# Kernel optimization log

Measured on AMD Instinct MI355X. Metric: run time of the kernel, lower is better.

The kernel has to match this reference:

```python
import jax, jax.numpy as jnp
import numpy as np

RADIUS = 5
WIN = (RADIUS - 1) * 2 + 1  # 9


def setup_inputs() -> dict:
    key = jax.random.key(0)
    k1, k2 = jax.random.split(key)
    B, K, H, W = 4, 4, 224, 224
    seg = jax.random.uniform(k1, (B, K, H, W), dtype=jnp.float32)
    weight = jax.random.uniform(k2, (B, 1, H, W, WIN, WIN), dtype=jnp.float32)
    return {"seg": seg, "weight": weight}


def reference(seg, weight):
    # seg: [B,K,H,W]; weight: [B,1,H,W,w,w] local affinity window, w = 2*(radius-1)+1
    B, K, H, W = seg.shape
    Kconst = jnp.float32(K)
    # torch pads by `radius` on all sides but only uses window offsets 0..2*(radius-1),
    # i.e. relative offsets [-radius, radius-2] -- replicate exactly.
    padded = jnp.pad(seg, ((0, 0), (0, 0), (RADIUS, RADIUS), (RADIUS, RADIUS)))
    # weighted sum over the local window without materializing [B,K,H,W,w,w]
    sum_w_seg = jnp.zeros_like(seg)
    for m in range(WIN):
        for n in range(WIN):
            sum_w_seg = sum_w_seg + padded[:, :, m:m + H, n:n + W] * weight[:, :, :, :, m, n]
    assocA = jnp.sum(sum_w_seg * seg, axis=(-1, -2))                      # [B,K]
    assocV = jnp.sum(jnp.sum(weight, axis=(-1, -2)) * seg, axis=(-1, -2))  # [B,K]
    assoc = jnp.sum(assocA / assocV, axis=-1)                              # [B]
    return jnp.sum(Kconst - assoc)
```

## Files before the change

### kernel.cpp

```cpp
#include <hip/hip_runtime.h>

#define RADIUS 5
#define WIN 9
#define BB 4
#define KK 4
#define HH 224
#define WW 224
#define HW (HH * WW)
#define PD 234
#define PAREA (PD * PD)
#define NBUCKET 64
#define PARTIAL_FLOATS (NBUCKET * BB * 8)
#define BLOCKS_PER_B (HW / 64)
#define TOTAL_BLOCKS (BB * BLOCKS_PER_B)


__global__ __launch_bounds__(256) void ncuts_pad(
    const float* __restrict__ seg, float4* __restrict__ pseg, float* __restrict__ zr)
{
    const int tid = blockIdx.x * 256 + threadIdx.x;
    if (tid < PARTIAL_FLOATS) zr[tid] = 0.f;
    if (tid >= BB * PAREA) return;
    const int b  = tid / PAREA;
    const int rc = tid - b * PAREA;
    const int r  = rc / PD;
    const int c  = rc - r * PD;
    const int hh = r - RADIUS;
    const int ww = c - RADIUS;
    float4 v = {0.f, 0.f, 0.f, 0.f};
    if (hh >= 0 && hh < HH && ww >= 0 && ww < WW) {
        const float* sb = seg + (size_t)b * KK * HW + hh * WW + ww;
        v.x = sb[0 * HW];
        v.y = sb[1 * HW];
        v.z = sb[2 * HW];
        v.w = sb[3 * HW];
    }
    pseg[tid] = v;
}

__global__ __launch_bounds__(64) void ncuts_main(
    const float* __restrict__ weight,
    const float4* __restrict__ pseg,
    float* __restrict__ partial)
{
    __shared__ float wlds[64 * 81];

    const int lane = threadIdx.x;
    const int tid  = blockIdx.x * 64 + lane;
    const int b    = tid / HW;
    const int rem  = tid - b * HW;
    const int h    = rem / WW;
    const int w    = rem - h * WW;

    const float4* wsrc = (const float4*)(weight + (size_t)blockIdx.x * (64 * 81));
    float4* ldsb = (float4*)wlds;
    #pragma unroll
    for (int j = 0; j < 20; ++j)
        __builtin_amdgcn_global_load_lds(
            (__attribute__((address_space(1))) void*)(wsrc + j * 64 + lane),
            (__attribute__((address_space(3))) void*)(ldsb + j * 64),
            16, 0, 0);
    if (lane < 16)
        __builtin_amdgcn_global_load_lds(
            (__attribute__((address_space(1))) void*)(wsrc + 1280 + lane),
            (__attribute__((address_space(3))) void*)(ldsb + 1280),
            16, 0, 0);

    const float4* p4 = pseg + (size_t)b * PAREA;
    const float4 t = p4[(h + RADIUS) * PD + (w + RADIUS)];

    __syncthreads();

    const float* wl = &wlds[lane * 81];

    float a0 = 0.f, a1 = 0.f, a2 = 0.f, a3 = 0.f, wsum = 0.f;

    #pragma unroll
    for (int m = 0; m < WIN; ++m) {
        const int base = (h + m) * PD + w;
        #pragma unroll
        for (int n = 0; n < WIN; ++n) {
            const float wv = wl[m * WIN + n];
            const float4 s = p4[base + n];
            a0 = fmaf(wv, s.x, a0);
            a1 = fmaf(wv, s.y, a1);
            a2 = fmaf(wv, s.z, a2);
            a3 = fmaf(wv, s.w, a3);
            wsum += wv;
        }
    }

    float vals[8] = { a0 * t.x, a1 * t.y, a2 * t.z, a3 * t.w,
                      wsum * t.x, wsum * t.y, wsum * t.z, wsum * t.w };

    #pragma unroll
    for (int i = 0; i < 8; ++i) {
        float v = vals[i];
        v += __shfl_down(v, 32);
        v += __shfl_down(v, 16);
        v += __shfl_down(v, 8);
        v += __shfl_down(v, 4);
        v += __shfl_down(v, 2);
        v += __shfl_down(v, 1);
        vals[i] = v;
    }

    if (lane == 0) {
        const int bb     = blockIdx.x - b * BLOCKS_PER_B;
        const int bucket = bb & (NBUCKET - 1);
        float* dst = partial + (bucket * BB + b) * 8;
        #pragma unroll
        for (int i = 0; i < 8; ++i)
            atomicAdd(dst + i, vals[i]);
    }
}

__global__ __launch_bounds__(64) void ncuts_final(
    const float* __restrict__ partial, float* __restrict__ out)
{
    __shared__ float sums[32];
    const int t = threadIdx.x;
    if (t < 32) {
        float s = 0.f;
        for (int bucket = 0; bucket < NBUCKET; ++bucket)
            s += partial[bucket * 32 + t];
        sums[t] = s;
    }
    __syncthreads();
    if (t == 0) {
        float total = 0.f;
        for (int b = 0; b < BB; ++b) {
            float assoc = 0.f;
            for (int k = 0; k < KK; ++k) {
                const float A = sums[b * 8 + k];
                const float V = sums[b * 8 + 4 + k];
                assoc += A / V;
            }
            total += (float)KK - assoc;
        }
        out[0] = total;
    }
}

extern "C" void kernel_launch(void* const* d_in, const int* in_sizes, int n_in,
                              void* d_out, int out_size, void* d_ws, size_t ws_size,
                              hipStream_t stream) {
    const float* seg    = (const float*)d_in[0];
    const float* weight = (const float*)d_in[1];
    float* out     = (float*)d_out;
    float* wsf     = (float*)d_ws;
    float* partial = wsf;
    float4* pseg   = (float4*)(wsf + PARTIAL_FLOATS);

    {
        const int total = BB * PAREA;
        const int grid  = (total + 255) / 256;
        hipLaunchKernelGGL(ncuts_pad, dim3(grid), dim3(256), 0, stream, seg, pseg, wsf);
    }

    hipLaunchKernelGGL(ncuts_main, dim3(TOTAL_BLOCKS), dim3(64), 0, stream,
                       weight, pseg, partial);

    hipLaunchKernelGGL(ncuts_final, dim3(1), dim3(64), 0, stream, partial, out);
}
```

Baseline: 105.7 us.

## Stream weight elements linearly per lane instead of staging per-pixel windows in LDS

The main kernel now treats the weight tensor as a flat stream: each lane reads one float per step with fully coalesced accesses and derives the pixel and window offset by incremental index tracking, instead of staging each pixel's 81 weights in LDS. The center seg value is folded into each weight before accumulation, so both numerator and denominator sums are built per element. Blocks grow to 4 waves, each covering 28 steps of 64 elements. The aim is to drop LDS staging and the barrier and to make the dominant weight read purely sequential. In exchange every step does two gather loads of seg (center and neighbor), recomputes the window offset with a divide by 9, and runs a branchy index update.

Result: slower. 114.8 us (+8.6%).

```diff
diff --git a/kernel.cpp b/kernel.cpp
--- a/kernel.cpp
+++ b/kernel.cpp
@@ -11,7 +11,12 @@
 #define PAREA (PD * PD)
 #define NBUCKET 64
 #define PARTIAL_FLOATS (NBUCKET * BB * 8)
-#define BLOCKS_PER_B (HW / 64)
+#define ELEMS_PER_B (HW * 81)
+#define STEPS 28
+#define WAVE_ELEMS (64 * STEPS)
+#define BLOCK_WAVES 4
+#define BLOCK_ELEMS (BLOCK_WAVES * WAVE_ELEMS)
+#define BLOCKS_PER_B (ELEMS_PER_B / BLOCK_ELEMS)
 #define TOTAL_BLOCKS (BB * BLOCKS_PER_B)
 
 
@@ -38,61 +43,60 @@
     pseg[tid] = v;
 }
 
-__global__ __launch_bounds__(64) void ncuts_main(
+__global__ __launch_bounds__(256) void ncuts_main(
     const float* __restrict__ weight,
     const float4* __restrict__ pseg,
     float* __restrict__ partial)
 {
-    __shared__ float wlds[64 * 81];
+    const int lane = threadIdx.x & 63;
+    const int wid  = threadIdx.x >> 6;
+    const int b    = blockIdx.x / BLOCKS_PER_B;
+    const int blkb = blockIdx.x - b * BLOCKS_PER_B;
 
-    const int lane = threadIdx.x;
-    const int tid  = blockIdx.x * 64 + lane;
-    const int b    = tid / HW;
-    const int rem  = tid - b * HW;
-    const int h    = rem / WW;
-    const int w    = rem - h * WW;
+    const unsigned wave_base = (unsigned)(blkb * BLOCK_WAVES + wid) * WAVE_ELEMS;
+    const unsigned idx0 = wave_base + (unsigned)lane;
 
-    const float4* wsrc = (const float4*)(weight + (size_t)blockIdx.x * (64 * 81));
-    float4* ldsb = (float4*)wlds;
-    #pragma unroll
-    for (int j = 0; j < 20; ++j)
-        __builtin_amdgcn_global_load_lds(
-            (__attribute__((address_space(1))) void*)(wsrc + j * 64 + lane),
-            (__attribute__((address_space(3))) void*)(ldsb + j * 64),
-            16, 0, 0);
-    if (lane < 16)
-        __builtin_amdgcn_global_load_lds(
-            (__attribute__((address_space(1))) void*)(wsrc + 1280 + lane),
-            (__attribute__((address_space(3))) void*)(ldsb + 1280),
-            16, 0, 0);
+    const float*  wsrc = weight + (size_t)b * ELEMS_PER_B;
+    const float4* p4   = pseg   + (size_t)b * PAREA;
 
-    const float4* p4 = pseg + (size_t)b * PAREA;
-    const float4 t = p4[(h + RADIUS) * PD + (w + RADIUS)];
+    unsigned p = idx0 / 81u;
+    unsigned o = idx0 - p * 81u;
+    unsigned h = p / 224u;
+    unsigned w = p - h * 224u;
 
-    __syncthreads();
-
-    const float* wl = &wlds[lane * 81];
-
-    float a0 = 0.f, a1 = 0.f, a2 = 0.f, a3 = 0.f, wsum = 0.f;
+    float a0 = 0.f, a1 = 0.f, a2 = 0.f, a3 = 0.f;
+    float v0 = 0.f, v1 = 0.f, v2 = 0.f, v3 = 0.f;
 
     #pragma unroll
-    for (int m = 0; m < WIN; ++m) {
-        const int base = (h + m) * PD + w;
-        #pragma unroll
-        for (int n = 0; n < WIN; ++n) {
-            const float wv = wl[m * WIN + n];
-            const float4 s = p4[base + n];
-            a0 = fmaf(wv, s.x, a0);
-            a1 = fmaf(wv, s.y, a1);
-            a2 = fmaf(wv, s.z, a2);
-            a3 = fmaf(wv, s.w, a3);
-            wsum += wv;
+    for (int j = 0; j < STEPS; ++j) {
+        const float wv = wsrc[wave_base + j * 64 + lane];
+
+        const unsigned m = o / 9u;
+        const unsigned n = o - m * 9u;
+
+        const float4 sc = p4[(h + RADIUS) * PD + (w + RADIUS)];
+        const float4 sv = p4[(h + m) * PD + (w + n)];
+
+        const float w0 = wv * sc.x;
+        const float w1 = wv * sc.y;
+        const float w2 = wv * sc.z;
+        const float w3 = wv * sc.w;
+
+        a0 = fmaf(w0, sv.x, a0);
+        a1 = fmaf(w1, sv.y, a1);
+        a2 = fmaf(w2, sv.z, a2);
+        a3 = fmaf(w3, sv.w, a3);
+        v0 += w0; v1 += w1; v2 += w2; v3 += w3;
+
+        o += 64u;
+        if (o >= 81u) {
+            o -= 81u;
+            ++w;
+            if (w == 224u) { w = 0u; ++h; }
         }
     }
 
-    float vals[8] = { a0 * t.x, a1 * t.y, a2 * t.z, a3 * t.w,
-                      wsum * t.x, wsum * t.y, wsum * t.z, wsum * t.w };
-
+    float vals[8] = { a0, a1, a2, a3, v0, v1, v2, v3 };
     #pragma unroll
     for (int i = 0; i < 8; ++i) {
         float v = vals[i];
@@ -106,8 +110,7 @@
     }
 
     if (lane == 0) {
-        const int bb     = blockIdx.x - b * BLOCKS_PER_B;
-        const int bucket = bb & (NBUCKET - 1);
+        const int bucket = (blkb + wid * 16) & (NBUCKET - 1);
         float* dst = partial + (bucket * BB + b) * 8;
         #pragma unroll
         for (int i = 0; i < 8; ++i)
@@ -158,7 +161,7 @@
         hipLaunchKernelGGL(ncuts_pad, dim3(grid), dim3(256), 0, stream, seg, pseg, wsf);
     }
 
-    hipLaunchKernelGGL(ncuts_main, dim3(TOTAL_BLOCKS), dim3(64), 0, stream,
+    hipLaunchKernelGGL(ncuts_main, dim3(TOTAL_BLOCKS), dim3(256), 0, stream,
                        weight, pseg, partial);
 
     hipLaunchKernelGGL(ncuts_final, dim3(1), dim3(64), 0, stream, partial, out);
```

## Process multiple row tiles per wave with double-buffered async LDS staging

Applied to the files above, without the earlier changes.

Each 64-lane block now handles seven 56-pixel row-segment tiles. It double-buffers both the weight window and a 9x64 padded seg patch in LDS using global_load_lds, with manual vmcnt waits, so the next tile's loads overlap the current tile's FMAs. Seg neighbours are read from LDS instead of global/L1, and the atomic reductions drop by a factor of seven. In exchange, 8 of 64 lanes sit idle, each block uses more LDS, there are fewer blocks in flight, and correctness depends on the hand-counted waitcnt values.

Measured after the change: 109.9 us. 4.0% more time.

```diff
diff --git a/kernel.cpp b/kernel.cpp
--- a/kernel.cpp
+++ b/kernel.cpp
@@ -11,8 +11,18 @@
 #define PAREA (PD * PD)
 #define NBUCKET 64
 #define PARTIAL_FLOATS (NBUCKET * BB * 8)
-#define BLOCKS_PER_B (HW / 64)
-#define TOTAL_BLOCKS (BB * BLOCKS_PER_B)
+
+#define TILE_PIX 56
+#define TILES_PER_B (HH * 4)
+#define TOTAL_TILES (BB * TILES_PER_B)
+#define TPB 7
+#define NBLK (TOTAL_TILES / TPB)
+#define TW_FLOATS (TILE_PIX * 81)
+#define TW_BYTES (TW_FLOATS * 4)
+#define TW_FULL_LOADS 17
+#define TW_REM 46
+#define TP_BYTES (9 * 64 * 16)
+#define LDS_BYTES (2 * TW_BYTES + 2 * TP_BYTES)
 
 
 __global__ __launch_bounds__(256) void ncuts_pad(
@@ -43,56 +53,96 @@
     const float4* __restrict__ pseg,
     float* __restrict__ partial)
 {
-    __shared__ float wlds[64 * 81];
+    __shared__ char lds[LDS_BYTES];
 
     const int lane = threadIdx.x;
-    const int tid  = blockIdx.x * 64 + lane;
-    const int b    = tid / HW;
-    const int rem  = tid - b * HW;
-    const int h    = rem / WW;
-    const int w    = rem - h * WW;
-
-    const float4* wsrc = (const float4*)(weight + (size_t)blockIdx.x * (64 * 81));
-    float4* ldsb = (float4*)wlds;
-    #pragma unroll
-    for (int j = 0; j < 20; ++j)
-        __builtin_amdgcn_global_load_lds(
-            (__attribute__((address_space(1))) void*)(wsrc + j * 64 + lane),
-            (__attribute__((address_space(3))) void*)(ldsb + j * 64),
-            16, 0, 0);
-    if (lane < 16)
-        __builtin_amdgcn_global_load_lds(
-            (__attribute__((address_space(1))) void*)(wsrc + 1280 + lane),
-            (__attribute__((address_space(3))) void*)(ldsb + 1280),
-            16, 0, 0);
-
+    const int blk  = blockIdx.x;
+    const int t0   = blk * TPB;
+    const int b    = t0 / TILES_PER_B;
     const float4* p4 = pseg + (size_t)b * PAREA;
-    const float4 t = p4[(h + RADIUS) * PD + (w + RADIUS)];
-
-    __syncthreads();
-
-    const float* wl = &wlds[lane * 81];
-
-    float a0 = 0.f, a1 = 0.f, a2 = 0.f, a3 = 0.f, wsum = 0.f;
-
-    #pragma unroll
-    for (int m = 0; m < WIN; ++m) {
-        const int base = (h + m) * PD + w;
+
+    auto stage_w = [&](int t, int s) {
+        const float4* src = (const float4*)(weight + (size_t)t * TW_FLOATS);
+        char* dst = lds + s * TW_BYTES;
         #pragma unroll
-        for (int n = 0; n < WIN; ++n) {
-            const float wv = wl[m * WIN + n];
-            const float4 s = p4[base + n];
-            a0 = fmaf(wv, s.x, a0);
-            a1 = fmaf(wv, s.y, a1);
-            a2 = fmaf(wv, s.z, a2);
-            a3 = fmaf(wv, s.w, a3);
-            wsum += wv;
+        for (int j = 0; j < TW_FULL_LOADS; ++j)
+            __builtin_amdgcn_global_load_lds(
+                (__attribute__((address_space(1))) void*)(src + j * 64 + lane),
+                (__attribute__((address_space(3))) void*)(dst + j * 1024),
+                16, 0, 0);
+        if (lane < TW_REM)
+            __builtin_amdgcn_global_load_lds(
+                (__attribute__((address_space(1))) void*)(src + TW_FULL_LOADS * 64 + lane),
+                (__attribute__((address_space(3))) void*)(dst + TW_FULL_LOADS * 1024),
+                16, 0, 0);
+    };
+    auto stage_p = [&](int t, int s) {
+        const int r  = t - b * TILES_PER_B;
+        const int h  = r >> 2;
+        const int w0 = (r & 3) * TILE_PIX;
+        const float4* src = p4 + h * PD + w0;
+        char* dst = lds + 2 * TW_BYTES + s * TP_BYTES;
+        #pragma unroll
+        for (int rr = 0; rr < 9; ++rr)
+            __builtin_amdgcn_global_load_lds(
+                (__attribute__((address_space(1))) void*)(src + rr * PD + lane),
+                (__attribute__((address_space(3))) void*)(dst + rr * 1024),
+                16, 0, 0);
+    };
+
+    stage_w(t0 + 0, 0);
+    stage_p(t0 + 0, 0);
+    stage_w(t0 + 1, 1);
+    stage_p(t0 + 1, 1);
+
+    float accA0 = 0.f, accA1 = 0.f, accA2 = 0.f, accA3 = 0.f;
+    float accV0 = 0.f, accV1 = 0.f, accV2 = 0.f, accV3 = 0.f;
+
+    for (int i = 0; i < TPB; ++i) {
+        if (i < TPB - 1) asm volatile("s_waitcnt vmcnt(27)" ::: "memory");
+        else             asm volatile("s_waitcnt vmcnt(0)"  ::: "memory");
+        __builtin_amdgcn_sched_barrier(0);
+
+        const int s = i & 1;
+        const float*  wl = (const float*)(lds + s * TW_BYTES) + lane * 81;
+        const float4* pl = (const float4*)(lds + 2 * TW_BYTES + s * TP_BYTES) + lane;
+
+        if (lane < TILE_PIX) {
+            float a0 = 0.f, a1 = 0.f, a2 = 0.f, a3 = 0.f, ws = 0.f;
+            #pragma unroll
+            for (int m = 0; m < WIN; ++m) {
+                #pragma unroll
+                for (int n = 0; n < WIN; ++n) {
+                    const float  wv = wl[m * WIN + n];
+                    const float4 sv = pl[m * 64 + n];
+                    a0 = fmaf(wv, sv.x, a0);
+                    a1 = fmaf(wv, sv.y, a1);
+                    a2 = fmaf(wv, sv.z, a2);
+                    a3 = fmaf(wv, sv.w, a3);
+                    ws += wv;
+                }
+            }
+            const float4 sc = pl[5 * 64 + 5];
+            accA0 = fmaf(a0, sc.x, accA0);
+            accA1 = fmaf(a1, sc.y, accA1);
+            accA2 = fmaf(a2, sc.z, accA2);
+            accA3 = fmaf(a3, sc.w, accA3);
+            accV0 = fmaf(ws, sc.x, accV0);
+            accV1 = fmaf(ws, sc.y, accV1);
+            accV2 = fmaf(ws, sc.z, accV2);
+            accV3 = fmaf(ws, sc.w, accV3);
         }
-    }
-
-    float vals[8] = { a0 * t.x, a1 * t.y, a2 * t.z, a3 * t.w,
-                      wsum * t.x, wsum * t.y, wsum * t.z, wsum * t.w };
-
+
+        if (i + 2 < TPB) {
+            __builtin_amdgcn_sched_barrier(0);
+            asm volatile("s_waitcnt lgkmcnt(0)" ::: "memory");
+            __builtin_amdgcn_sched_barrier(0);
+            stage_w(t0 + i + 2, s);
+            stage_p(t0 + i + 2, s);
+        }
+    }
+
+    float vals[8] = { accA0, accA1, accA2, accA3, accV0, accV1, accV2, accV3 };
     #pragma unroll
     for (int i = 0; i < 8; ++i) {
         float v = vals[i];
@@ -104,10 +154,8 @@
         v += __shfl_down(v, 1);
         vals[i] = v;
     }
-
     if (lane == 0) {
-        const int bb     = blockIdx.x - b * BLOCKS_PER_B;
-        const int bucket = bb & (NBUCKET - 1);
+        const int bucket = blk & (NBUCKET - 1);
         float* dst = partial + (bucket * BB + b) * 8;
         #pragma unroll
         for (int i = 0; i < 8; ++i)
@@ -158,7 +206,7 @@
         hipLaunchKernelGGL(ncuts_pad, dim3(grid), dim3(256), 0, stream, seg, pseg, wsf);
     }
 
-    hipLaunchKernelGGL(ncuts_main, dim3(TOTAL_BLOCKS), dim3(64), 0, stream,
+    hipLaunchKernelGGL(ncuts_main, dim3(NBLK), dim3(64), 0, stream,
                        weight, pseg, partial);
 
     hipLaunchKernelGGL(ncuts_final, dim3(1), dim3(64), 0, stream, partial, out);
```

## Split each pixel's window across two lanes with 32-pixel row segments per block

Applied to the files above, without the earlier changes.

Each 64-lane block now covers 32 pixels of one row instead of 64 pixels, and each pixel's 9x9 window is split between two lanes by even and odd column offsets. This doubles the number of blocks and halves the LDS staged per block, which is meant to raise occupancy and shorten each lane's serial FMA and load chain. The cost is twice as many blocks, wave-level reductions and atomics, plus a lane-divergent ninth column.

Result: slower. 115.6 us (+9.3%).

```diff
diff --git a/kernel.cpp b/kernel.cpp
--- a/kernel.cpp
+++ b/kernel.cpp
@@ -11,8 +11,15 @@
 #define PAREA (PD * PD)
 #define NBUCKET 64
 #define PARTIAL_FLOATS (NBUCKET * BB * 8)
-#define BLOCKS_PER_B (HW / 64)
-#define TOTAL_BLOCKS (BB * BLOCKS_PER_B)
+
+#define SEGPIX 32
+#define SEGS_PER_ROW 7
+#define SEGS_PER_B (HH * SEGS_PER_ROW)
+#define NBLK (BB * SEGS_PER_B)
+#define WSEG_FLOATS (SEGPIX * 81)
+#define WSEG_BYTES (WSEG_FLOATS * 4)
+#define WSEG_FULL 10
+#define WSEG_REM_LANES 8
 
 
 __global__ __launch_bounds__(256) void ncuts_pad(
@@ -43,55 +50,67 @@
     const float4* __restrict__ pseg,
     float* __restrict__ partial)
 {
-    __shared__ float wlds[64 * 81];
+    __shared__ float wlds[WSEG_FLOATS];
 
     const int lane = threadIdx.x;
-    const int tid  = blockIdx.x * 64 + lane;
-    const int b    = tid / HW;
-    const int rem  = tid - b * HW;
-    const int h    = rem / WW;
-    const int w    = rem - h * WW;
+    const int blk  = blockIdx.x;
+    const int b    = blk / SEGS_PER_B;
+    const int sb   = blk - b * SEGS_PER_B;
+    const int h    = sb / SEGS_PER_ROW;
+    const int w0   = (sb - h * SEGS_PER_ROW) * SEGPIX;
+    const int q    = lane >> 1;
+    const int z    = lane & 1;
 
-    const float4* wsrc = (const float4*)(weight + (size_t)blockIdx.x * (64 * 81));
+    const float4* wsrc = (const float4*)(weight + (size_t)blk * WSEG_FLOATS);
     float4* ldsb = (float4*)wlds;
     #pragma unroll
-    for (int j = 0; j < 20; ++j)
+    for (int j = 0; j < WSEG_FULL; ++j)
         __builtin_amdgcn_global_load_lds(
             (__attribute__((address_space(1))) void*)(wsrc + j * 64 + lane),
             (__attribute__((address_space(3))) void*)(ldsb + j * 64),
             16, 0, 0);
-    if (lane < 16)
+    if (lane < WSEG_REM_LANES)
         __builtin_amdgcn_global_load_lds(
-            (__attribute__((address_space(1))) void*)(wsrc + 1280 + lane),
-            (__attribute__((address_space(3))) void*)(ldsb + 1280),
+            (__attribute__((address_space(1))) void*)(wsrc + WSEG_FULL * 64 + lane),
+            (__attribute__((address_space(3))) void*)(ldsb + WSEG_FULL * 64),
             16, 0, 0);
 
     const float4* p4 = pseg + (size_t)b * PAREA;
-    const float4 t = p4[(h + RADIUS) * PD + (w + RADIUS)];
+    const float4 t = p4[(h + RADIUS) * PD + (w0 + q + RADIUS)];
 
     __syncthreads();
 
-    const float* wl = &wlds[lane * 81];
+    const float* wl = wlds + q * 81;
 
-    float a0 = 0.f, a1 = 0.f, a2 = 0.f, a3 = 0.f, wsum = 0.f;
+    float a0 = 0.f, a1 = 0.f, a2 = 0.f, a3 = 0.f, ws = 0.f;
 
     #pragma unroll
     for (int m = 0; m < WIN; ++m) {
-        const int base = (h + m) * PD + w;
+        const int rowbase = (h + m) * PD + w0 + q;
         #pragma unroll
-        for (int n = 0; n < WIN; ++n) {
-            const float wv = wl[m * WIN + n];
-            const float4 s = p4[base + n];
-            a0 = fmaf(wv, s.x, a0);
-            a1 = fmaf(wv, s.y, a1);
-            a2 = fmaf(wv, s.z, a2);
-            a3 = fmaf(wv, s.w, a3);
-            wsum += wv;
+        for (int j = 0; j < 4; ++j) {
+            const int n = 2 * j + z;
+            const float  wv = wl[m * WIN + n];
+            const float4 sv = p4[rowbase + n];
+            a0 = fmaf(wv, sv.x, a0);
+            a1 = fmaf(wv, sv.y, a1);
+            a2 = fmaf(wv, sv.z, a2);
+            a3 = fmaf(wv, sv.w, a3);
+            ws += wv;
+        }
+        if (z == 0) {
+            const float  wv = wl[m * WIN + 8];
+            const float4 sv = p4[rowbase + 8];
+            a0 = fmaf(wv, sv.x, a0);
+            a1 = fmaf(wv, sv.y, a1);
+            a2 = fmaf(wv, sv.z, a2);
+            a3 = fmaf(wv, sv.w, a3);
+            ws += wv;
         }
     }
 
     float vals[8] = { a0 * t.x, a1 * t.y, a2 * t.z, a3 * t.w,
-                      wsum * t.x, wsum * t.y, wsum * t.z, wsum * t.w };
+                      ws * t.x, ws * t.y, ws * t.z, ws * t.w };
 
     #pragma unroll
     for (int i = 0; i < 8; ++i) {
@@ -106,8 +125,7 @@
     }
 
     if (lane == 0) {
-        const int bb     = blockIdx.x - b * BLOCKS_PER_B;
-        const int bucket = bb & (NBUCKET - 1);
+        const int bucket = sb & (NBUCKET - 1);
         float* dst = partial + (bucket * BB + b) * 8;
         #pragma unroll
         for (int i = 0; i < 8; ++i)
@@ -158,7 +176,7 @@
         hipLaunchKernelGGL(ncuts_pad, dim3(grid), dim3(256), 0, stream, seg, pseg, wsf);
     }
 
-    hipLaunchKernelGGL(ncuts_main, dim3(TOTAL_BLOCKS), dim3(64), 0, stream,
+    hipLaunchKernelGGL(ncuts_main, dim3(NBLK), dim3(64), 0, stream,
                        weight, pseg, partial);
 
     hipLaunchKernelGGL(ncuts_final, dim3(1), dim3(64), 0, stream, partial, out);
```
